# Performance work log

Measured on AMD Instinct MI355X. Metric: run time of the kernel, lower is better.

## Reference

```python
import jax, jax.numpy as jnp
import numpy as np

L, D, FF, V, B, S, H, GS = 6, 1024, 4096, 32000, 2, 1024, 16, 128
DH = D // H


def setup_inputs() -> dict:
    key = jax.random.key(0)
    ks = jax.random.split(key, 32)

    def tern(k, shape):
        # ternary values in {-1, 0, 1}, stored as float32 (int8 buffer in torch)
        return jax.random.randint(k, shape, -1, 2).astype(jnp.float32)

    def sc(k, shape):
        # positive per-group scales (abs-mean init, clamped > 0)
        return jax.random.uniform(k, shape, jnp.float32, 0.01, 0.1)

    inp = {
        'input_ids': jax.random.randint(ks[0], (B, S), 0, V),
        'emb_t': tern(ks[1], (V, D)),
        'emb_s': sc(ks[2], (V * D // GS,)),
        'pos_emb': jax.random.normal(ks[3], (S, D), jnp.float32) * 0.02,
        'q_t': tern(ks[4], (L, D, D)), 'q_s': sc(ks[5], (L, D * D // GS)),
        'k_t': tern(ks[6], (L, D, D)), 'k_s': sc(ks[7], (L, D * D // GS)),
        'v_t': tern(ks[8], (L, D, D)), 'v_s': sc(ks[9], (L, D * D // GS)),
        'o_t': tern(ks[10], (L, D, D)), 'o_s': sc(ks[11], (L, D * D // GS)),
        'g_t': tern(ks[12], (L, FF, D)), 'g_s': sc(ks[13], (L, D * FF // GS)),
        'u_t': tern(ks[14], (L, FF, D)), 'u_s': sc(ks[15], (L, D * FF // GS)),
        'd_t': tern(ks[16], (L, D, FF)), 'd_s': sc(ks[17], (L, D * FF // GS)),
        'alpha': jnp.full((L, H, 1, 1), 0.1, jnp.float32),
        'na_w': jnp.ones((L, D), jnp.float32),
        'nm_w': jnp.ones((L, D), jnp.float32),
        'nf_w': jnp.ones((D,), jnp.float32),
        'head_t': tern(ks[18], (V, D)),
        'head_s': sc(ks[19], (V * D // GS,)),
    }
    return inp


def _dq(t, s):
    # dequantize: reshape ternary to (..., n_groups, GS), scale per group
    tg = t.reshape(t.shape[:-2] + (-1, GS))
    return (tg * s[..., :, None]).reshape(t.shape)


def _rms(x, w, eps=1e-6):
    return x * jax.lax.rsqrt(jnp.mean(x * x, axis=-1, keepdims=True) + eps) * w


def _forward(input_ids, emb_t, emb_s, pos_emb, q_t, q_s, k_t, k_s, v_t, v_s,
             o_t, o_s, g_t, g_s, u_t, u_s, d_t, d_s, alpha, na_w, nm_w, nf_w,
             head_t, head_s):
    x = _dq(emb_t, emb_s)[input_ids] + pos_emb[None, :S]  # [B,S,D]
    causal = jnp.tril(jnp.ones((S, S), bool))
    scale = DH ** -0.5

    def block(x, p):
        (qt, qs, kt, ks_, vt, vs, ot, os_, gt, gs_, ut, us, dt, ds,
         al, naw, nmw) = p
        h = _rms(x, naw)

        def proj(t, s):
            return (h @ _dq(t, s).T).reshape(B, S, H, DH).transpose(0, 2, 1, 3)

        q, k, v = proj(qt, qs), proj(kt, ks_), proj(vt, vs)
        att = jnp.einsum('bhqd,bhkd->bhqk', q, k) * scale
        att = jax.nn.softmax(jnp.where(causal, att, -jnp.inf), axis=-1)
        out = jnp.einsum('bhqk,bhkd->bhqd', att, v)
        # residual head-mix: out += alpha * x_heads (x here is the normed input h)
        out = out + al * h.reshape(B, S, H, DH).transpose(0, 2, 1, 3)
        out = out.transpose(0, 2, 1, 3).reshape(B, S, D)
        x = x + out @ _dq(ot, os_).T
        h2 = _rms(x, nmw)
        gate = h2 @ _dq(gt, gs_).T
        up = h2 @ _dq(ut, us).T
        x = x + (jax.nn.silu(gate) * up) @ _dq(dt, ds).T
        return x, None

    params = (q_t, q_s, k_t, k_s, v_t, v_s, o_t, o_s, g_t, g_s, u_t, u_s,
              d_t, d_s, alpha, na_w, nm_w)
    x, _ = jax.lax.scan(block, x, params)
    x = _rms(x, nf_w)
    return x @ _dq(head_t, head_s).T  # [B,S,V]


def reference(input_ids, emb_t, emb_s, pos_emb, q_t, q_s, k_t, k_s, v_t, v_s,
              o_t, o_s, g_t, g_s, u_t, u_s, d_t, d_s, alpha, na_w, nm_w, nf_w,
              head_t, head_s):
    return _forward(input_ids, emb_t, emb_s, pos_emb, q_t, q_s, k_t, k_s,
                    v_t, v_s, o_t, o_s, g_t, g_s, u_t, u_s, d_t, d_s,
                    alpha, na_w, nm_w, nf_w, head_t, head_s)
```

## Files before the change

kernel.cpp:

```cpp
#include <hip/hip_runtime.h>
#include <math.h>

#define Lc   6
#define Dc   1024
#define FFc  4096
#define Vc   32000
#define Bc   2
#define Sc   1024
#define Hc   16
#define GSc  128
#define DHc  64
#define Mc   (Bc * Sc)

typedef __attribute__((ext_vector_type(8))) short bf16x8;
typedef __attribute__((ext_vector_type(4))) float f32x4;

__device__ inline unsigned ph2(float a, float b) {
    return (__float_as_uint(b) & 0xffff0000u) | (__float_as_uint(a) >> 16);
}
__device__ inline float flo(float a) {
    return a - __uint_as_float(__float_as_uint(a) & 0xffff0000u);
}
__device__ inline ushort bhi(float a) { return (ushort)(__float_as_uint(a) >> 16); }
__device__ inline ushort blo(float a) { return (ushort)(__float_as_uint(flo(a)) >> 16); }
__device__ inline float unbf(ushort h) { return __uint_as_float((unsigned)h << 16); }

__device__ inline size_t swz_bidx(int row, int col, int K) {
    size_t byte = (size_t)col * 2;
    size_t base = (size_t)row * K * 2 + (byte & ~(size_t)127);
    int inner = (int)(byte & 127);
    inner = (inner & 15) | ((((inner >> 4) ^ (row & 7)) & 7) << 4);
    return base + (size_t)inner;
}

__device__ inline void glds16(const void* g, void* l) {
    __builtin_amdgcn_global_load_lds(
        (const __attribute__((address_space(1))) void*)g,
        (__attribute__((address_space(3))) void*)l, 16, 0, 0);
}

__device__ inline float block_reduce_sum(float v, float* scratch) {
    __syncthreads();
    int lane = threadIdx.x & 63, w = threadIdx.x >> 6;
#pragma unroll
    for (int off = 32; off > 0; off >>= 1) v += __shfl_down(v, off, 64);
    if (lane == 0) scratch[w] = v;
    __syncthreads();
    if (threadIdx.x == 0) scratch[0] = scratch[0] + scratch[1] + scratch[2] + scratch[3];
    __syncthreads();
    return scratch[0];
}

__global__ __launch_bounds__(256) void k_embed(const int* __restrict__ ids,
                                               const float* __restrict__ et,
                                               const float* __restrict__ es,
                                               const float* __restrict__ pos,
                                               float* __restrict__ x) {
    int row = blockIdx.x;
    int sp  = row & (Sc - 1);
    int d   = threadIdx.x << 2;
    int idx = ids[row];
    int base = idx * Dc + d;
    float4 t = *(const float4*)(et + base);
    float  s = es[base >> 7];
    float4 p = *(const float4*)(pos + sp * Dc + d);
    float4 o;
    o.x = fmaf(t.x, s, p.x); o.y = fmaf(t.y, s, p.y);
    o.z = fmaf(t.z, s, p.z); o.w = fmaf(t.w, s, p.w);
    *(float4*)(x + row * Dc + d) = o;
}

__global__ __launch_bounds__(256) void k_rmsnorm_bf(const float* __restrict__ x,
                                                    const float* __restrict__ w,
                                                    ushort* __restrict__ hi,
                                                    ushort* __restrict__ lo) {
    __shared__ float scratch[4];
    int row = blockIdx.x;
    int d = threadIdx.x << 2;
    float4 f = *(const float4*)(x + (size_t)row * Dc + d);
    float s = f.x * f.x + f.y * f.y + f.z * f.z + f.w * f.w;
    s = block_reduce_sum(s, scratch);
    float rinv = rsqrtf(s * (1.0f / Dc) + 1e-6f);
    float4 wv = *(const float4*)(w + d);
    float o0 = f.x * rinv * wv.x, o1 = f.y * rinv * wv.y;
    float o2 = f.z * rinv * wv.z, o3 = f.w * rinv * wv.w;
    ushort4 hv, lv;
    hv.x = bhi(o0); hv.y = bhi(o1); hv.z = bhi(o2); hv.w = bhi(o3);
    lv.x = blo(o0); lv.y = blo(o1); lv.z = blo(o2); lv.w = blo(o3);
    const size_t sb = swz_bidx(row, d, Dc);
    *(ushort4*)((char*)hi + sb) = hv;
    *(ushort4*)((char*)lo + sb) = lv;
}

template <bool RESID>
__device__ __forceinline__ void gemm_core(
    const ushort* __restrict__ Ahi, const ushort* __restrict__ Alo,
    const float* __restrict__ Wt, const float* __restrict__ Ws,
    const float* __restrict__ R, float* __restrict__ C,
    const int bn, const int N, const int K, const int g0, const int g1) {
    __shared__ char Ah[16384];
    __shared__ char Al[16384];
    __shared__ char Bh[16384];
    __shared__ float Wsl[128];

    const int tid  = threadIdx.x;
    const int lane = tid & 63;
    const int wv   = tid >> 6;
    const int wm   = (wv >> 1) << 6;
    const int wn   = (wv & 1) << 6;
    const int bm   = blockIdx.x << 7;
    const int kg   = K >> 7;

    const int sr   = tid >> 1;
    const int sh   = tid & 1;
    const int swr  = (sr & 7) << 4;
    const int rowb = sr << 7;
    const int colb = sh << 6;
    const float* Bbase = Wt + (size_t)(bn + sr) * K + (sh << 5);

    const int gr = (wv << 3) + (lane >> 3);
    const int gc = (lane & 7) << 4;
    const char* Abh = (const char*)Ahi;
    const char* Abl = (const char*)Alo;

    const int lr  = lane & 15;
    const int lkb = (lane >> 4) << 4;
    const int frs = (lane & 7) << 4;

    f32x4 acc[4][4], accg[4][4];
#pragma unroll
    for (int i = 0; i < 4; ++i)
#pragma unroll
        for (int j = 0; j < 4; ++j) {
            acc[i][j]  = (f32x4){0.f, 0.f, 0.f, 0.f};
            accg[i][j] = (f32x4){0.f, 0.f, 0.f, 0.f};
        }

    float4 bv[8];
    const int s0 = g0 << 1, s1 = g1 << 1;
    {
        const float4* p = (const float4*)(Bbase + (s0 << 6));
#pragma unroll
        for (int jj = 0; jj < 8; ++jj) bv[jj] = p[jj];
    }

    for (int s = s0; s < s1; ++s) {
        const int k0 = s << 6;
        __syncthreads();
#pragma unroll
        for (int i = 0; i < 4; ++i) {
            const size_t sb = ((size_t)(bm + gr + (i << 5)) * K + k0) * 2 + gc;
            glds16(Abh + sb, Ah + (wv << 10) + (i << 12));
            glds16(Abl + sb, Al + (wv << 10) + (i << 12));
        }
        if ((s & 1) == 0 && tid < 128)
            Wsl[tid] = Ws[(size_t)(bn + tid) * kg + (s >> 1)];
#pragma unroll
        for (int j = 0; j < 4; ++j) {
            const int ob = rowb + ((colb + (j << 4)) ^ swr);
            float4 x0 = bv[2 * j], x1 = bv[2 * j + 1];
            *(uint4*)(Bh + ob) = make_uint4(ph2(x0.x, x0.y), ph2(x0.z, x0.w),
                                            ph2(x1.x, x1.y), ph2(x1.z, x1.w));
        }
        __syncthreads();
        if (s + 1 < s1) {
            const float4* p = (const float4*)(Bbase + ((s + 1) << 6));
#pragma unroll
            for (int jj = 0; jj < 8; ++jj) bv[jj] = p[jj];
        }
#pragma unroll
        for (int ks = 0; ks < 2; ++ks) {
            bf16x8 fa[4], fl[4], fb[4];
            const int cb = ((ks << 6) + lkb) ^ frs;
#pragma unroll
            for (int f = 0; f < 4; ++f) {
                const int ra = (wm + (f << 4) + lr) << 7;
                fa[f] = *(const bf16x8*)(Ah + ra + cb);
                fl[f] = *(const bf16x8*)(Al + ra + cb);
                const int rb = (wn + (f << 4) + lr) << 7;
                fb[f] = *(const bf16x8*)(Bh + rb + cb);
            }
#pragma unroll
            for (int i = 0; i < 4; ++i)
#pragma unroll
                for (int j = 0; j < 4; ++j) {
                    accg[i][j] = __builtin_amdgcn_mfma_f32_16x16x32_bf16(fa[i], fb[j], accg[i][j], 0, 0, 0);
                    accg[i][j] = __builtin_amdgcn_mfma_f32_16x16x32_bf16(fl[i], fb[j], accg[i][j], 0, 0, 0);
                }
        }
        if (s & 1) {
            float sv[4];
#pragma unroll
            for (int j = 0; j < 4; ++j) sv[j] = Wsl[wn + (j << 4) + lr];
#pragma unroll
            for (int i = 0; i < 4; ++i)
#pragma unroll
                for (int j = 0; j < 4; ++j) {
                    acc[i][j] += accg[i][j] * sv[j];
                    accg[i][j] = (f32x4){0.f, 0.f, 0.f, 0.f};
                }
        }
    }

    const int r0 = bm + wm + ((lane >> 4) << 2);
    const int c0 = bn + wn + lr;
#pragma unroll
    for (int i = 0; i < 4; ++i) {
        const int row = r0 + (i << 4);
#pragma unroll
        for (int j = 0; j < 4; ++j) {
            size_t off = (size_t)row * N + c0 + (j << 4);
#pragma unroll
            for (int e = 0; e < 4; ++e) {
                float vv = acc[i][j][e];
                if (RESID) vv += R[off];
                C[off] = vv;
                off += (size_t)N;
            }
        }
    }
}

template <bool RESID>
__global__ __launch_bounds__(256, 2) void k_gemm_bfa(
    const ushort* __restrict__ Ahi, const ushort* __restrict__ Alo,
    const float* __restrict__ Wt, const float* __restrict__ Ws,
    const float* __restrict__ R, float* __restrict__ C, int N, int K) {
    gemm_core<RESID>(Ahi, Alo, Wt, Ws, R, C, blockIdx.y << 7, N, K, 0, K >> 7);
}

__global__ __launch_bounds__(256, 2) void k_gemm_part(
    const ushort* __restrict__ Ahi, const ushort* __restrict__ Alo,
    const float* __restrict__ Wt, const float* __restrict__ Ws,
    float* __restrict__ P, int N, int K, int gper) {
    const int z = blockIdx.z;
    gemm_core<false>(Ahi, Alo, Wt, Ws, nullptr, P + (size_t)z * Mc * Dc,
                     blockIdx.y << 7, N, K, z * gper, (z + 1) * gper);
}

__global__ __launch_bounds__(256, 2) void k_gemm_qkv(
    const ushort* __restrict__ Ahi, const ushort* __restrict__ Alo,
    const float* __restrict__ qt, const float* __restrict__ qs,
    const float* __restrict__ kt, const float* __restrict__ ks,
    const float* __restrict__ vt, const float* __restrict__ vs,
    float* __restrict__ qb, float* __restrict__ kb, float* __restrict__ vb) {
    const int which = blockIdx.y >> 3;
    const int bn = (blockIdx.y & 7) << 7;
    const float* Wt = which == 0 ? qt : which == 1 ? kt : vt;
    const float* Ws = which == 0 ? qs : which == 1 ? ks : vs;
    float* C = which == 0 ? qb : which == 1 ? kb : vb;
    gemm_core<false>(Ahi, Alo, Wt, Ws, nullptr, C, bn, Dc, Dc, 0, Dc >> 7);
}

__global__ __launch_bounds__(256, 2) void k_gemm_gu(
    const ushort* __restrict__ Ahi, const ushort* __restrict__ Alo,
    const float* __restrict__ gt, const float* __restrict__ gs,
    const float* __restrict__ ut, const float* __restrict__ us,
    float* __restrict__ gate, float* __restrict__ up) {
    const int which = blockIdx.y >> 5;
    const int bn = (blockIdx.y & 31) << 7;
    const float* Wt = which == 0 ? gt : ut;
    const float* Ws = which == 0 ? gs : us;
    float* C = which == 0 ? gate : up;
    gemm_core<false>(Ahi, Alo, Wt, Ws, nullptr, C, bn, FFc, Dc, 0, Dc >> 7);
}

__global__ __launch_bounds__(256) void k_red4(const float* __restrict__ p,
                                              float* __restrict__ x) {
    const size_t i = (((size_t)blockIdx.x << 8) + threadIdx.x) << 2;
    const size_t st = (size_t)Mc * Dc;
    float4 a  = *(const float4*)(x + i);
    float4 p0 = *(const float4*)(p + i);
    float4 p1 = *(const float4*)(p + i + st);
    float4 p2 = *(const float4*)(p + i + 2 * st);
    float4 p3 = *(const float4*)(p + i + 3 * st);
    a.x += p0.x + p1.x + p2.x + p3.x;
    a.y += p0.y + p1.y + p2.y + p3.y;
    a.z += p0.z + p1.z + p2.z + p3.z;
    a.w += p0.w + p1.w + p2.w + p3.w;
    *(float4*)(x + i) = a;
}

__global__ __launch_bounds__(256) void k_silumul(const float* __restrict__ g,
                                                 const float* __restrict__ u,
                                                 ushort* __restrict__ fhi,
                                                 ushort* __restrict__ fl2) {
    const size_t i = (((size_t)blockIdx.x << 8) + threadIdx.x) << 2;
    float4 gv = *(const float4*)(g + i);
    float4 uv = *(const float4*)(u + i);
    float r0 = uv.x * (gv.x / (1.0f + expf(-gv.x)));
    float r1 = uv.y * (gv.y / (1.0f + expf(-gv.y)));
    float r2 = uv.z * (gv.z / (1.0f + expf(-gv.z)));
    float r3 = uv.w * (gv.w / (1.0f + expf(-gv.w)));
    ushort4 hv, lv;
    hv.x = bhi(r0); hv.y = bhi(r1); hv.z = bhi(r2); hv.w = bhi(r3);
    lv.x = blo(r0); lv.y = blo(r1); lv.z = blo(r2); lv.w = blo(r3);
    const int row = (int)(i >> 12);
    const int col = (int)(i & 4095);
    const size_t sb = swz_bidx(row, col, FFc);
    *(ushort4*)((char*)fhi + sb) = hv;
    *(ushort4*)((char*)fl2 + sb) = lv;
}

__global__ __launch_bounds__(256, 2) void k_attn_mfma(
    const float* __restrict__ q, const float* __restrict__ k,
    const float* __restrict__ v, const ushort* __restrict__ hnhi,
    const ushort* __restrict__ hnlo, const float* __restrict__ alpha,
    ushort* __restrict__ aohi, ushort* __restrict__ aolo) {
    __shared__ uint4 KhV[512], KlV[512];
    __shared__ uint4 VthV[512], VtlV[512];
    __shared__ uint4 PhV[512], PlV[512];
    char* Khc  = (char*)KhV;
    char* Klc  = (char*)KlV;
    char* Vthc = (char*)VthV;
    char* Vtlc = (char*)VtlV;

    const int t = blockIdx.x, hh = blockIdx.y, b = blockIdx.z;
    const int tid  = threadIdx.x;
    const int lane = tid & 63, w = tid >> 6;
    const int lr = lane & 15, g = lane >> 4;
    const int bS = b * Sc;
    const int hoff = hh * DHc;

    char* myPh = (char*)PhV + (w << 11);
    char* myPl = (char*)PlV + (w << 11);

    const int qrow = (t << 6) + (w << 4) + lr;
    bf16x8 qh[2], ql[2];
    {
        const float* qp = q + (size_t)(bS + qrow) * Dc + hoff + (g << 3);
#pragma unroll
        for (int c = 0; c < 2; ++c) {
            float4 f0 = *(const float4*)(qp + (c << 5));
            float4 f1 = *(const float4*)(qp + (c << 5) + 4);
            float s[8] = {f0.x * 0.125f, f0.y * 0.125f, f0.z * 0.125f, f0.w * 0.125f,
                          f1.x * 0.125f, f1.y * 0.125f, f1.z * 0.125f, f1.w * 0.125f};
            union { bf16x8 v; unsigned u[4]; } Hh, Ll;
#pragma unroll
            for (int p = 0; p < 4; ++p) {
                Hh.u[p] = ph2(s[2 * p], s[2 * p + 1]);
                Ll.u[p] = ph2(flo(s[2 * p]), flo(s[2 * p + 1]));
            }
            qh[c] = Hh.v; ql[c] = Ll.v;
        }
    }

    f32x4 oacc[4];
    float m[4], lsum[4];
#pragma unroll
    for (int f = 0; f < 4; ++f) oacc[f] = (f32x4){0.f, 0.f, 0.f, 0.f};
#pragma unroll
    for (int e = 0; e < 4; ++e) { m[e] = -3.0e38f; lsum[e] = 0.f; }

    const int skey = tid >> 2, sseg = tid & 3;
    const int k4 = (tid >> 4) << 2, d4 = (tid & 15) << 2;

    float4 kr[4], vr[4];
    {
        const float* src = k + (size_t)(bS + skey) * Dc + hoff + (sseg << 4);
#pragma unroll
        for (int r = 0; r < 4; ++r) kr[r] = *(const float4*)(src + (r << 2));
        const float* vsrc = v + (size_t)(bS + k4) * Dc + hoff + d4;
#pragma unroll
        for (int r = 0; r < 4; ++r) vr[r] = *(const float4*)(vsrc + r * Dc);
    }

    const int nt = t + 1;
    for (int j = 0; j < nt; ++j) {
        {
            const int swz = (skey & 7) << 4;
            char* dsth = Khc + skey * 128;
            char* dstl = Klc + skey * 128;
            float4 a0 = kr[0], a1 = kr[1], a2 = kr[2], a3 = kr[3];
            *(uint4*)(dsth + (((sseg << 5)) ^ swz)) =
                make_uint4(ph2(a0.x, a0.y), ph2(a0.z, a0.w), ph2(a1.x, a1.y), ph2(a1.z, a1.w));
            *(uint4*)(dsth + (((sseg << 5) + 16) ^ swz)) =
                make_uint4(ph2(a2.x, a2.y), ph2(a2.z, a2.w), ph2(a3.x, a3.y), ph2(a3.z, a3.w));
            *(uint4*)(dstl + (((sseg << 5)) ^ swz)) =
                make_uint4(ph2(flo(a0.x), flo(a0.y)), ph2(flo(a0.z), flo(a0.w)),
                           ph2(flo(a1.x), flo(a1.y)), ph2(flo(a1.z), flo(a1.w)));
            *(uint4*)(dstl + (((sseg << 5) + 16) ^ swz)) =
                make_uint4(ph2(flo(a2.x), flo(a2.y)), ph2(flo(a2.z), flo(a2.w)),
                           ph2(flo(a3.x), flo(a3.y)), ph2(flo(a3.z), flo(a3.w)));
        }
        {
            union { float4 v4; float f[4]; } r0, r1, r2, r3;
            r0.v4 = vr[0]; r1.v4 = vr[1]; r2.v4 = vr[2]; r3.v4 = vr[3];
#pragma unroll
            for (int d = 0; d < 4; ++d) {
                const int dh = d4 + d;
                const int byt = dh * 128 + (((k4 << 1)) ^ ((dh & 7) << 4));
                float x0 = r0.f[d], x1 = r1.f[d], x2 = r2.f[d], x3 = r3.f[d];
                *(uint2*)(Vthc + byt) = make_uint2(ph2(x0, x1), ph2(x2, x3));
                *(uint2*)(Vtlc + byt) =
                    make_uint2(ph2(flo(x0), flo(x1)), ph2(flo(x2), flo(x3)));
            }
        }
        __syncthreads();
        if (j + 1 < nt) {
            const int kb2 = (j + 1) << 6;
            const float* src = k + (size_t)(bS + kb2 + skey) * Dc + hoff + (sseg << 4);
#pragma unroll
            for (int r = 0; r < 4; ++r) kr[r] = *(const float4*)(src + (r << 2));
            const float* vsrc = v + (size_t)(bS + kb2 + k4) * Dc + hoff + d4;
#pragma unroll
            for (int r = 0; r < 4; ++r) vr[r] = *(const float4*)(vsrc + r * Dc);
        }

        f32x4 sacc[4];
#pragma unroll
        for (int f = 0; f < 4; ++f) sacc[f] = (f32x4){0.f, 0.f, 0.f, 0.f};
#pragma unroll
        for (int c = 0; c < 2; ++c) {
            const int cb = (c << 6) + (g << 4);
#pragma unroll
            for (int f = 0; f < 4; ++f) {
                const int row = (f << 4) + lr;
                const int byt = row * 128 + (cb ^ ((row & 7) << 4));
                bf16x8 kh = *(const bf16x8*)(Khc + byt);
                bf16x8 kl = *(const bf16x8*)(Klc + byt);
                sacc[f] = __builtin_amdgcn_mfma_f32_16x16x32_bf16(qh[c], kh, sacc[f], 0, 0, 0);
                sacc[f] = __builtin_amdgcn_mfma_f32_16x16x32_bf16(ql[c], kh, sacc[f], 0, 0, 0);
                sacc[f] = __builtin_amdgcn_mfma_f32_16x16x32_bf16(qh[c], kl, sacc[f], 0, 0, 0);
            }
        }
        if (j == t) {
            const int qloc = (w << 4) + (g << 2);
#pragma unroll
            for (int f = 0; f < 4; ++f) {
                const int key = (f << 4) + lr;
#pragma unroll
                for (int e = 0; e < 4; ++e)
                    if (key > qloc + e) sacc[f][e] = -3.0e38f;
            }
        }
        float rmax[4], corr[4], rsum[4];
#pragma unroll
        for (int e = 0; e < 4; ++e)
            rmax[e] = fmaxf(fmaxf(sacc[0][e], sacc[1][e]), fmaxf(sacc[2][e], sacc[3][e]));
#pragma unroll
        for (int msk = 1; msk <= 8; msk <<= 1)
#pragma unroll
            for (int e = 0; e < 4; ++e)
                rmax[e] = fmaxf(rmax[e], __shfl_xor(rmax[e], msk, 64));
#pragma unroll
        for (int e = 0; e < 4; ++e) {
            float mn = fmaxf(m[e], rmax[e]);
            corr[e] = __expf(m[e] - mn);
            m[e] = mn;
            rsum[e] = 0.f;
        }
#pragma unroll
        for (int f = 0; f < 4; ++f)
#pragma unroll
            for (int e = 0; e < 4; ++e) {
                float p = __expf(sacc[f][e] - m[e]);
                sacc[f][e] = p;
                rsum[e] += p;
            }
#pragma unroll
        for (int msk = 1; msk <= 8; msk <<= 1)
#pragma unroll
            for (int e = 0; e < 4; ++e) rsum[e] += __shfl_xor(rsum[e], msk, 64);
#pragma unroll
        for (int e = 0; e < 4; ++e) lsum[e] = lsum[e] * corr[e] + rsum[e];
#pragma unroll
        for (int f = 0; f < 4; ++f)
#pragma unroll
            for (int e = 0; e < 4; ++e) oacc[f][e] *= corr[e];

#pragma unroll
        for (int f = 0; f < 4; ++f) {
            const int key2 = ((f << 4) + lr) << 1;
#pragma unroll
            for (int e = 0; e < 4; ++e) {
                const int qr = (g << 2) + e;
                const int byt = qr * 128 + (key2 ^ ((qr & 7) << 4));
                unsigned bits = __float_as_uint(sacc[f][e]);
                unsigned hib = bits & 0xffff0000u;
                *(short*)(myPh + byt) = (short)(hib >> 16);
                float lov = sacc[f][e] - __uint_as_float(hib);
                *(short*)(myPl + byt) = (short)(__float_as_uint(lov) >> 16);
            }
        }
#pragma unroll
        for (int c = 0; c < 2; ++c) {
            const int cb = (c << 6) + (g << 4);
            const int pbyt = lr * 128 + (cb ^ ((lr & 7) << 4));
            bf16x8 pah = *(const bf16x8*)(myPh + pbyt);
            bf16x8 pal = *(const bf16x8*)(myPl + pbyt);
#pragma unroll
            for (int f = 0; f < 4; ++f) {
                const int row = (f << 4) + lr;
                const int byt = row * 128 + (cb ^ ((row & 7) << 4));
                bf16x8 vbh = *(const bf16x8*)(Vthc + byt);
                bf16x8 vbl = *(const bf16x8*)(Vtlc + byt);
                oacc[f] = __builtin_amdgcn_mfma_f32_16x16x32_bf16(pah, vbh, oacc[f], 0, 0, 0);
                oacc[f] = __builtin_amdgcn_mfma_f32_16x16x32_bf16(pal, vbh, oacc[f], 0, 0, 0);
                oacc[f] = __builtin_amdgcn_mfma_f32_16x16x32_bf16(pah, vbl, oacc[f], 0, 0, 0);
            }
        }
        __syncthreads();
    }

    const float al = alpha[hh];
    float invl[4];
#pragma unroll
    for (int e = 0; e < 4; ++e) invl[e] = 1.0f / lsum[e];
#pragma unroll
    for (int f = 0; f < 4; ++f) {
        const int dh = (f << 4) + lr;
#pragma unroll
        for (int e = 0; e < 4; ++e) {
            const int qg = (t << 6) + (w << 4) + (g << 2) + e;
            const int row = bS + qg;
            const size_t sb = swz_bidx(row, hoff + dh, Dc);
            float hnv = unbf(*(const ushort*)((const char*)hnhi + sb)) +
                        unbf(*(const ushort*)((const char*)hnlo + sb));
            float val = fmaf(al, hnv, oacc[f][e] * invl[e]);
            *(ushort*)((char*)aohi + sb) = bhi(val);
            *(ushort*)((char*)aolo + sb) = blo(val);
        }
    }
}

extern "C" void kernel_launch(void* const* d_in, const int* in_sizes, int n_in,
                              void* d_out, int out_size, void* d_ws, size_t ws_size,
                              hipStream_t stream) {
    const int*   ids    = (const int*)d_in[0];
    const float* emb_t  = (const float*)d_in[1];
    const float* emb_s  = (const float*)d_in[2];
    const float* pos    = (const float*)d_in[3];
    const float* q_t    = (const float*)d_in[4];
    const float* q_s    = (const float*)d_in[5];
    const float* k_t    = (const float*)d_in[6];
    const float* k_s    = (const float*)d_in[7];
    const float* v_t    = (const float*)d_in[8];
    const float* v_s    = (const float*)d_in[9];
    const float* o_t    = (const float*)d_in[10];
    const float* o_s    = (const float*)d_in[11];
    const float* g_t    = (const float*)d_in[12];
    const float* g_s    = (const float*)d_in[13];
    const float* u_t    = (const float*)d_in[14];
    const float* u_s    = (const float*)d_in[15];
    const float* dd_t   = (const float*)d_in[16];
    const float* dd_s   = (const float*)d_in[17];
    const float* alpha  = (const float*)d_in[18];
    const float* na_w   = (const float*)d_in[19];
    const float* nm_w   = (const float*)d_in[20];
    const float* nf_w   = (const float*)d_in[21];
    const float* head_t = (const float*)d_in[22];
    const float* head_s = (const float*)d_in[23];
    float* outp = (float*)d_out;

    float*  ws   = (float*)d_ws;
    float*  x    = ws;
    ushort* hhi  = (ushort*)(x + (size_t)Mc * Dc);
    ushort* hlo  = hhi + (size_t)Mc * Dc;
    float*  big  = (float*)(hlo + (size_t)Mc * Dc);
    float*  qb   = big;
    float*  kb   = big + (size_t)Mc * Dc;
    float*  vb   = big + (size_t)2 * Mc * Dc;
    ushort* aohi = (ushort*)(big + (size_t)3 * Mc * Dc);
    ushort* aolo = aohi + (size_t)Mc * Dc;
    float*  up   = big;
    float*  gate = (float*)d_out;
    ushort* ffhi = (ushort*)((char*)d_out + (size_t)Mc * FFc * 4);
    ushort* fflo = ffhi + (size_t)Mc * FFc;

    k_embed<<<Mc, 256, 0, stream>>>(ids, emb_t, emb_s, pos, x);

    const dim3 gD(Mc / 128, Dc / 128);
    const dim3 gQKV(Mc / 128, 3 * Dc / 128);
    const dim3 gGU(Mc / 128, 2 * FFc / 128);
    const dim3 gDN(Mc / 128, Dc / 128, 4);
    const dim3 gH(Mc / 128, Vc / 128);
    const dim3 gA(Sc / 64, Hc, Bc);
    const int  gSilu = (Mc * FFc) / (256 * 4);
    const int  gRed  = (Mc * Dc) / (256 * 4);

    for (int l = 0; l < Lc; ++l) {
        const float* qt = q_t + (size_t)l * Dc * Dc;
        const float* qs = q_s + (size_t)l * (Dc * Dc / GSc);
        const float* kt = k_t + (size_t)l * Dc * Dc;
        const float* ks = k_s + (size_t)l * (Dc * Dc / GSc);
        const float* vt = v_t + (size_t)l * Dc * Dc;
        const float* vs = v_s + (size_t)l * (Dc * Dc / GSc);
        const float* ot = o_t + (size_t)l * Dc * Dc;
        const float* os = o_s + (size_t)l * (Dc * Dc / GSc);
        const float* gt = g_t + (size_t)l * FFc * Dc;
        const float* gs = g_s + (size_t)l * (FFc * Dc / GSc);
        const float* ut = u_t + (size_t)l * FFc * Dc;
        const float* us = u_s + (size_t)l * (FFc * Dc / GSc);
        const float* dt = dd_t + (size_t)l * Dc * FFc;
        const float* ds = dd_s + (size_t)l * (Dc * FFc / GSc);

        k_rmsnorm_bf<<<Mc, 256, 0, stream>>>(x, na_w + l * Dc, hhi, hlo);
        k_gemm_qkv<<<gQKV, 256, 0, stream>>>(hhi, hlo, qt, qs, kt, ks, vt, vs, qb, kb, vb);
        k_attn_mfma<<<gA, 256, 0, stream>>>(qb, kb, vb, hhi, hlo, alpha + l * Hc, aohi, aolo);
        k_gemm_bfa<true><<<gD, 256, 0, stream>>>(aohi, aolo, ot, os, x, x, Dc, Dc);
        k_rmsnorm_bf<<<Mc, 256, 0, stream>>>(x, nm_w + l * Dc, hhi, hlo);
        k_gemm_gu<<<gGU, 256, 0, stream>>>(hhi, hlo, gt, gs, ut, us, gate, up);
        k_silumul<<<gSilu, 256, 0, stream>>>(gate, up, ffhi, fflo);
        k_gemm_part<<<gDN, 256, 0, stream>>>(ffhi, fflo, dt, ds, big, Dc, FFc, 8);
        k_red4<<<gRed, 256, 0, stream>>>(big, x);
    }

    k_rmsnorm_bf<<<Mc, 256, 0, stream>>>(x, nf_w, hhi, hlo);
    k_gemm_bfa<false><<<gH, 256, 0, stream>>>(hhi, hlo, head_t, head_s, nullptr, outp, Vc, Dc);
}
```

Measured before the change: 3.144 ms.

## Double-buffer GEMM LDS with 128x256 tiles, 512 threads and swizzled block order

Rewrites the shared GEMM core to use 512-thread blocks computing 128x256 tiles, with double-buffered LDS for A and B so the next k-step's loads overlap the current MFMA work and only one barrier is needed per step. Group scales are read directly into registers instead of through LDS, and a block-index swizzle reorders tiles to improve L2 reuse. The output projection now uses split-K partials plus the existing reduction kernel instead of a fused residual epilogue. The larger LDS footprint limits occupancy and adds an extra reduction pass for the O projection.

```diff
diff --git a/kernel.cpp b/kernel.cpp
--- a/kernel.cpp
+++ b/kernel.cpp
@@ -37,6 +37,15 @@
     __builtin_amdgcn_global_load_lds(
         (const __attribute__((address_space(1))) void*)g,
         (__attribute__((address_space(3))) void*)l, 16, 0, 0);
+}
+
+__device__ inline void swz_mt(int& m, int& t) {
+    const int nb  = gridDim.x * gridDim.y * gridDim.z;
+    const int bid = (blockIdx.z * gridDim.y + blockIdx.y) * gridDim.x + blockIdx.x;
+    const int q   = nb >> 3;
+    const int w   = (bid & 7) * q + (bid >> 3);
+    m = w & 15;
+    t = w >> 4;
 }
 
 __device__ inline float block_reduce_sum(float v, float* scratch) {
@@ -92,23 +101,21 @@
     *(ushort4*)((char*)lo + sb) = lv;
 }
 
-template <bool RESID>
-__device__ __forceinline__ void gemm_core(
+__device__ __forceinline__ void gemm_core2(
     const ushort* __restrict__ Ahi, const ushort* __restrict__ Alo,
     const float* __restrict__ Wt, const float* __restrict__ Ws,
-    const float* __restrict__ R, float* __restrict__ C,
-    const int bn, const int N, const int K, const int g0, const int g1) {
-    __shared__ char Ah[16384];
-    __shared__ char Al[16384];
-    __shared__ char Bh[16384];
-    __shared__ float Wsl[128];
+    float* __restrict__ C,
+    const int bm, const int bn, const int N, const int K,
+    const int g0, const int g1) {
+    __shared__ char AhB[32768];
+    __shared__ char AlB[32768];
+    __shared__ char BhB[65536];
 
     const int tid  = threadIdx.x;
     const int lane = tid & 63;
     const int wv   = tid >> 6;
-    const int wm   = (wv >> 1) << 6;
-    const int wn   = (wv & 1) << 6;
-    const int bm   = blockIdx.x << 7;
+    const int wm   = (wv & 1) << 6;
+    const int wn   = (wv >> 1) << 6;
     const int kg   = K >> 7;
 
     const int sr   = tid >> 1;
@@ -118,15 +125,21 @@
     const int colb = sh << 6;
     const float* Bbase = Wt + (size_t)(bn + sr) * K + (sh << 5);
 
-    const int gr = (wv << 3) + (lane >> 3);
-    const int gc = (lane & 7) << 4;
+    const int gr = tid >> 3;
+    const int gc = (tid & 7) << 4;
     const char* Abh = (const char*)Ahi;
     const char* Abl = (const char*)Alo;
+    const size_t K2 = (size_t)K * 2;
 
     const int lr  = lane & 15;
     const int lkb = (lane >> 4) << 4;
     const int frs = (lane & 7) << 4;
 
+    const float* Wsp[4];
+#pragma unroll
+    for (int j = 0; j < 4; ++j)
+        Wsp[j] = Ws + (size_t)(bn + wn + (j << 4) + lr) * kg;
+
     f32x4 acc[4][4], accg[4][4];
 #pragma unroll
     for (int i = 0; i < 4; ++i)
@@ -136,62 +149,86 @@
             accg[i][j] = (f32x4){0.f, 0.f, 0.f, 0.f};
         }
 
+    const int s0 = g0 << 1, s1 = g1 << 1;
     float4 bv[8];
-    const int s0 = g0 << 1, s1 = g1 << 1;
+    float  sv[4];
+
     {
-        const float4* p = (const float4*)(Bbase + (s0 << 6));
+        const int k0 = s0 << 6;
+#pragma unroll
+        for (int i = 0; i < 2; ++i) {
+            const size_t sb = (size_t)(bm + (i << 6) + gr) * K2 + ((size_t)k0 << 1) + gc;
+            glds16(Abh + sb, AhB + (i << 13) + (wv << 10));
+            glds16(Abl + sb, AlB + (i << 13) + (wv << 10));
+        }
+        const float4* p = (const float4*)(Bbase + k0);
 #pragma unroll
         for (int jj = 0; jj < 8; ++jj) bv[jj] = p[jj];
-    }
-
-    for (int s = s0; s < s1; ++s) {
-        const int k0 = s << 6;
-        __syncthreads();
-#pragma unroll
-        for (int i = 0; i < 4; ++i) {
-            const size_t sb = ((size_t)(bm + gr + (i << 5)) * K + k0) * 2 + gc;
-            glds16(Abh + sb, Ah + (wv << 10) + (i << 12));
-            glds16(Abl + sb, Al + (wv << 10) + (i << 12));
-        }
-        if ((s & 1) == 0 && tid < 128)
-            Wsl[tid] = Ws[(size_t)(bn + tid) * kg + (s >> 1)];
 #pragma unroll
         for (int j = 0; j < 4; ++j) {
             const int ob = rowb + ((colb + (j << 4)) ^ swr);
             float4 x0 = bv[2 * j], x1 = bv[2 * j + 1];
-            *(uint4*)(Bh + ob) = make_uint4(ph2(x0.x, x0.y), ph2(x0.z, x0.w),
-                                            ph2(x1.x, x1.y), ph2(x1.z, x1.w));
-        }
-        __syncthreads();
+            *(uint4*)(BhB + ob) = make_uint4(ph2(x0.x, x0.y), ph2(x0.z, x0.w),
+                                             ph2(x1.x, x1.y), ph2(x1.z, x1.w));
+        }
+    }
+    __syncthreads();
+
+    int cur = 0;
+    for (int s = s0; s < s1; ++s) {
+        const int nxt = cur ^ 1;
         if (s + 1 < s1) {
-            const float4* p = (const float4*)(Bbase + ((s + 1) << 6));
+            const int k0 = (s + 1) << 6;
+#pragma unroll
+            for (int i = 0; i < 2; ++i) {
+                const size_t sb = (size_t)(bm + (i << 6) + gr) * K2 + ((size_t)k0 << 1) + gc;
+                glds16(Abh + sb, AhB + (nxt << 14) + (i << 13) + (wv << 10));
+                glds16(Abl + sb, AlB + (nxt << 14) + (i << 13) + (wv << 10));
+            }
+            const float4* p = (const float4*)(Bbase + k0);
 #pragma unroll
             for (int jj = 0; jj < 8; ++jj) bv[jj] = p[jj];
         }
+        if ((s & 1) == 0) {
+#pragma unroll
+            for (int j = 0; j < 4; ++j) sv[j] = Wsp[j][s >> 1];
+        }
+
+        const char* AhC = AhB + (cur << 14);
+        const char* AlC = AlB + (cur << 14);
+        const char* BhC = BhB + (cur << 15);
 #pragma unroll
         for (int ks = 0; ks < 2; ++ks) {
-            bf16x8 fa[4], fl[4], fb[4];
             const int cb = ((ks << 6) + lkb) ^ frs;
+            bf16x8 fa[4], fl[4];
 #pragma unroll
             for (int f = 0; f < 4; ++f) {
                 const int ra = (wm + (f << 4) + lr) << 7;
-                fa[f] = *(const bf16x8*)(Ah + ra + cb);
-                fl[f] = *(const bf16x8*)(Al + ra + cb);
-                const int rb = (wn + (f << 4) + lr) << 7;
-                fb[f] = *(const bf16x8*)(Bh + rb + cb);
-            }
-#pragma unroll
-            for (int i = 0; i < 4; ++i)
-#pragma unroll
-                for (int j = 0; j < 4; ++j) {
-                    accg[i][j] = __builtin_amdgcn_mfma_f32_16x16x32_bf16(fa[i], fb[j], accg[i][j], 0, 0, 0);
-                    accg[i][j] = __builtin_amdgcn_mfma_f32_16x16x32_bf16(fl[i], fb[j], accg[i][j], 0, 0, 0);
+                fa[f] = *(const bf16x8*)(AhC + ra + cb);
+                fl[f] = *(const bf16x8*)(AlC + ra + cb);
+            }
+#pragma unroll
+            for (int j = 0; j < 4; ++j) {
+                const int rb = (wn + (j << 4) + lr) << 7;
+                bf16x8 fb = *(const bf16x8*)(BhC + rb + cb);
+#pragma unroll
+                for (int i = 0; i < 4; ++i) {
+                    accg[i][j] = __builtin_amdgcn_mfma_f32_16x16x32_bf16(fa[i], fb, accg[i][j], 0, 0, 0);
+                    accg[i][j] = __builtin_amdgcn_mfma_f32_16x16x32_bf16(fl[i], fb, accg[i][j], 0, 0, 0);
                 }
+            }
+        }
+        if (s + 1 < s1) {
+            char* BhN = BhB + (nxt << 15);
+#pragma unroll
+            for (int j = 0; j < 4; ++j) {
+                const int ob = rowb + ((colb + (j << 4)) ^ swr);
+                float4 x0 = bv[2 * j], x1 = bv[2 * j + 1];
+                *(uint4*)(BhN + ob) = make_uint4(ph2(x0.x, x0.y), ph2(x0.z, x0.w),
+                                                 ph2(x1.x, x1.y), ph2(x1.z, x1.w));
+            }
         }
         if (s & 1) {
-            float sv[4];
-#pragma unroll
-            for (int j = 0; j < 4; ++j) sv[j] = Wsl[wn + (j << 4) + lr];
 #pragma unroll
             for (int i = 0; i < 4; ++i)
 #pragma unroll
@@ -200,6 +237,8 @@
                     accg[i][j] = (f32x4){0.f, 0.f, 0.f, 0.f};
                 }
         }
+        __syncthreads();
+        cur = nxt;
     }
 
     const int r0 = bm + wm + ((lane >> 4) << 2);
@@ -212,57 +251,58 @@
             size_t off = (size_t)row * N + c0 + (j << 4);
 #pragma unroll
             for (int e = 0; e < 4; ++e) {
-                float vv = acc[i][j][e];
-                if (RESID) vv += R[off];
-                C[off] = vv;
+                C[off] = acc[i][j][e];
                 off += (size_t)N;
             }
         }
     }
 }
 
-template <bool RESID>
-__global__ __launch_bounds__(256, 2) void k_gemm_bfa(
+__global__ __launch_bounds__(512, 2) void k_gemm_bfa(
     const ushort* __restrict__ Ahi, const ushort* __restrict__ Alo,
     const float* __restrict__ Wt, const float* __restrict__ Ws,
-    const float* __restrict__ R, float* __restrict__ C, int N, int K) {
-    gemm_core<RESID>(Ahi, Alo, Wt, Ws, R, C, blockIdx.y << 7, N, K, 0, K >> 7);
-}
-
-__global__ __launch_bounds__(256, 2) void k_gemm_part(
+    float* __restrict__ C, int N, int K) {
+    int m, t; swz_mt(m, t);
+    gemm_core2(Ahi, Alo, Wt, Ws, C, m << 7, t << 8, N, K, 0, K >> 7);
+}
+
+__global__ __launch_bounds__(512, 2) void k_gemm_part(
     const ushort* __restrict__ Ahi, const ushort* __restrict__ Alo,
     const float* __restrict__ Wt, const float* __restrict__ Ws,
-    float* __restrict__ P, int N, int K, int gper) {
-    const int z = blockIdx.z;
-    gemm_core<false>(Ahi, Alo, Wt, Ws, nullptr, P + (size_t)z * Mc * Dc,
-                     blockIdx.y << 7, N, K, z * gper, (z + 1) * gper);
-}
-
-__global__ __launch_bounds__(256, 2) void k_gemm_qkv(
+    float* __restrict__ P, int K, int gper) {
+    int m, t; swz_mt(m, t);
+    const int y = t & 3, z = t >> 2;
+    gemm_core2(Ahi, Alo, Wt, Ws, P + (size_t)z * Mc * Dc,
+               m << 7, y << 8, Dc, K, z * gper, (z + 1) * gper);
+}
+
+__global__ __launch_bounds__(512, 2) void k_gemm_qkv(
     const ushort* __restrict__ Ahi, const ushort* __restrict__ Alo,
     const float* __restrict__ qt, const float* __restrict__ qs,
     const float* __restrict__ kt, const float* __restrict__ ks,
     const float* __restrict__ vt, const float* __restrict__ vs,
     float* __restrict__ qb, float* __restrict__ kb, float* __restrict__ vb) {
-    const int which = blockIdx.y >> 3;
-    const int bn = (blockIdx.y & 7) << 7;
+    int m, t; swz_mt(m, t);
+    const int which = t >> 2;
+    const int bn = (t & 3) << 8;
     const float* Wt = which == 0 ? qt : which == 1 ? kt : vt;
     const float* Ws = which == 0 ? qs : which == 1 ? ks : vs;
     float* C = which == 0 ? qb : which == 1 ? kb : vb;
-    gemm_core<false>(Ahi, Alo, Wt, Ws, nullptr, C, bn, Dc, Dc, 0, Dc >> 7);
-}
-
-__global__ __launch_bounds__(256, 2) void k_gemm_gu(
+    gemm_core2(Ahi, Alo, Wt, Ws, C, m << 7, bn, Dc, Dc, 0, Dc >> 7);
+}
+
+__global__ __launch_bounds__(512, 2) void k_gemm_gu(
     const ushort* __restrict__ Ahi, const ushort* __restrict__ Alo,
     const float* __restrict__ gt, const float* __restrict__ gs,
     const float* __restrict__ ut, const float* __restrict__ us,
     float* __restrict__ gate, float* __restrict__ up) {
-    const int which = blockIdx.y >> 5;
-    const int bn = (blockIdx.y & 31) << 7;
+    int m, t; swz_mt(m, t);
+    const int which = t >> 4;
+    const int bn = (t & 15) << 8;
     const float* Wt = which == 0 ? gt : ut;
     const float* Ws = which == 0 ? gs : us;
     float* C = which == 0 ? gate : up;
-    gemm_core<false>(Ahi, Alo, Wt, Ws, nullptr, C, bn, FFc, Dc, 0, Dc >> 7);
+    gemm_core2(Ahi, Alo, Wt, Ws, C, m << 7, bn, FFc, Dc, 0, Dc >> 7);
 }
 
 __global__ __launch_bounds__(256) void k_red4(const float* __restrict__ p,
@@ -565,16 +605,16 @@
     ushort* aolo = aohi + (size_t)Mc * Dc;
     float*  up   = big;
     float*  gate = (float*)d_out;
+    float*  part = (float*)d_out;
     ushort* ffhi = (ushort*)((char*)d_out + (size_t)Mc * FFc * 4);
     ushort* fflo = ffhi + (size_t)Mc * FFc;
 
     k_embed<<<Mc, 256, 0, stream>>>(ids, emb_t, emb_s, pos, x);
 
-    const dim3 gD(Mc / 128, Dc / 128);
-    const dim3 gQKV(Mc / 128, 3 * Dc / 128);
-    const dim3 gGU(Mc / 128, 2 * FFc / 128);
-    const dim3 gDN(Mc / 128, Dc / 128, 4);
-    const dim3 gH(Mc / 128, Vc / 128);
+    const dim3 gQKV(Mc / 128, 12);
+    const dim3 gGU(Mc / 128, 32);
+    const dim3 gSK(Mc / 128, 4, 4);
+    const dim3 gH(Mc / 128, Vc / 256);
     const dim3 gA(Sc / 64, Hc, Bc);
     const int  gSilu = (Mc * FFc) / (256 * 4);
     const int  gRed  = (Mc * Dc) / (256 * 4);
@@ -596,16 +636,17 @@
         const float* ds = dd_s + (size_t)l * (Dc * FFc / GSc);
 
         k_rmsnorm_bf<<<Mc, 256, 0, stream>>>(x, na_w + l * Dc, hhi, hlo);
-        k_gemm_qkv<<<gQKV, 256, 0, stream>>>(hhi, hlo, qt, qs, kt, ks, vt, vs, qb, kb, vb);
+        k_gemm_qkv<<<gQKV, 512, 0, stream>>>(hhi, hlo, qt, qs, kt, ks, vt, vs, qb, kb, vb);
         k_attn_mfma<<<gA, 256, 0, stream>>>(qb, kb, vb, hhi, hlo, alpha + l * Hc, aohi, aolo);
-        k_gemm_bfa<true><<<gD, 256, 0, stream>>>(aohi, aolo, ot, os, x, x, Dc, Dc);
+        k_gemm_part<<<gSK, 512, 0, stream>>>(aohi, aolo, ot, os, part, Dc, 2);
+        k_red4<<<gRed, 256, 0, stream>>>(part, x);
         k_rmsnorm_bf<<<Mc, 256, 0, stream>>>(x, nm_w + l * Dc, hhi, hlo);
-        k_gemm_gu<<<gGU, 256, 0, stream>>>(hhi, hlo, gt, gs, ut, us, gate, up);
+        k_gemm_gu<<<gGU, 512, 0, stream>>>(hhi, hlo, gt, gs, ut, us, gate, up);
         k_silumul<<<gSilu, 256, 0, stream>>>(gate, up, ffhi, fflo);
-        k_gemm_part<<<gDN, 256, 0, stream>>>(ffhi, fflo, dt, ds, big, Dc, FFc, 8);
-        k_red4<<<gRed, 256, 0, stream>>>(big, x);
+        k_gemm_part<<<gSK, 512, 0, stream>>>(ffhi, fflo, dt, ds, part, FFc, 8);
+        k_red4<<<gRed, 256, 0, stream>>>(part, x);
     }
 
     k_rmsnorm_bf<<<Mc, 256, 0, stream>>>(x, nf_w, hhi, hlo);
-    k_gemm_bfa<false><<<gH, 256, 0, stream>>>(hhi, hlo, head_t, head_s, nullptr, outp, Vc, Dc);
-}
+    k_gemm_bfa<<<gH, 512, 0, stream>>>(hhi, hlo, head_t, head_s, outp, Vc, Dc);
+}
```

Result: slower. 3.589 ms (+14.2%).

## Swizzle GEMM block order, split-K the O-projection, raise occupancy to 3

Applied to the files above, without the earlier changes.

Adds a block-index remap that spreads consecutive block ids across chunks of the grid, so blocks running at the same time share weight tiles across the 16 M-tiles and L2 reuse improves. The O-projection now uses 4-way split-K partial GEMMs plus the reduce kernel instead of a single residual GEMM, which gives it more blocks to fill the GPU. Launch bounds go from 2 to 3 blocks per CU. The cost is extra partial-sum traffic and one more kernel launch per layer, plus tighter register limits that may cause spills.

```diff
diff --git a/kernel.cpp b/kernel.cpp
--- a/kernel.cpp
+++ b/kernel.cpp
@@ -37,6 +37,15 @@
     __builtin_amdgcn_global_load_lds(
         (const __attribute__((address_space(1))) void*)g,
         (__attribute__((address_space(3))) void*)l, 16, 0, 0);
+}
+
+__device__ inline void swz_mt(int& m, int& t) {
+    const int nb  = gridDim.x * gridDim.y * gridDim.z;
+    const int bid = (blockIdx.z * gridDim.y + blockIdx.y) * gridDim.x + blockIdx.x;
+    const int q   = nb >> 3;
+    const int w   = (bid & 7) * q + (bid >> 3);
+    m = w & 15;
+    t = w >> 4;
 }
 
 __device__ inline float block_reduce_sum(float v, float* scratch) {
@@ -97,7 +106,8 @@
     const ushort* __restrict__ Ahi, const ushort* __restrict__ Alo,
     const float* __restrict__ Wt, const float* __restrict__ Ws,
     const float* __restrict__ R, float* __restrict__ C,
-    const int bn, const int N, const int K, const int g0, const int g1) {
+    const int bm, const int bn, const int N, const int K,
+    const int g0, const int g1) {
     __shared__ char Ah[16384];
     __shared__ char Al[16384];
     __shared__ char Bh[16384];
@@ -108,7 +118,6 @@
     const int wv   = tid >> 6;
     const int wm   = (wv >> 1) << 6;
     const int wn   = (wv & 1) << 6;
-    const int bm   = blockIdx.x << 7;
     const int kg   = K >> 7;
 
     const int sr   = tid >> 1;
@@ -221,48 +230,51 @@
     }
 }
 
-template <bool RESID>
-__global__ __launch_bounds__(256, 2) void k_gemm_bfa(
+__global__ __launch_bounds__(256, 3) void k_gemm_head(
     const ushort* __restrict__ Ahi, const ushort* __restrict__ Alo,
     const float* __restrict__ Wt, const float* __restrict__ Ws,
-    const float* __restrict__ R, float* __restrict__ C, int N, int K) {
-    gemm_core<RESID>(Ahi, Alo, Wt, Ws, R, C, blockIdx.y << 7, N, K, 0, K >> 7);
-}
-
-__global__ __launch_bounds__(256, 2) void k_gemm_part(
+    float* __restrict__ C, int N, int K) {
+    int m, t; swz_mt(m, t);
+    gemm_core<false>(Ahi, Alo, Wt, Ws, nullptr, C, m << 7, t << 7, N, K, 0, K >> 7);
+}
+
+__global__ __launch_bounds__(256, 3) void k_gemm_part(
     const ushort* __restrict__ Ahi, const ushort* __restrict__ Alo,
     const float* __restrict__ Wt, const float* __restrict__ Ws,
-    float* __restrict__ P, int N, int K, int gper) {
-    const int z = blockIdx.z;
+    float* __restrict__ P, int K, int gper) {
+    int m, t; swz_mt(m, t);
+    const int y = t & 7, z = t >> 3;
     gemm_core<false>(Ahi, Alo, Wt, Ws, nullptr, P + (size_t)z * Mc * Dc,
-                     blockIdx.y << 7, N, K, z * gper, (z + 1) * gper);
-}
-
-__global__ __launch_bounds__(256, 2) void k_gemm_qkv(
+                     m << 7, y << 7, Dc, K, z * gper, (z + 1) * gper);
+}
+
+__global__ __launch_bounds__(256, 3) void k_gemm_qkv(
     const ushort* __restrict__ Ahi, const ushort* __restrict__ Alo,
     const float* __restrict__ qt, const float* __restrict__ qs,
     const float* __restrict__ kt, const float* __restrict__ ks,
     const float* __restrict__ vt, const float* __restrict__ vs,
     float* __restrict__ qb, float* __restrict__ kb, float* __restrict__ vb) {
-    const int which = blockIdx.y >> 3;
-    const int bn = (blockIdx.y & 7) << 7;
+    int m, t; swz_mt(m, t);
+    const int which = t >> 3;
+    const int bn = (t & 7) << 7;
     const float* Wt = which == 0 ? qt : which == 1 ? kt : vt;
     const float* Ws = which == 0 ? qs : which == 1 ? ks : vs;
     float* C = which == 0 ? qb : which == 1 ? kb : vb;
-    gemm_core<false>(Ahi, Alo, Wt, Ws, nullptr, C, bn, Dc, Dc, 0, Dc >> 7);
-}
-
-__global__ __launch_bounds__(256, 2) void k_gemm_gu(
+    gemm_core<false>(Ahi, Alo, Wt, Ws, nullptr, C, m << 7, bn, Dc, Dc, 0, Dc >> 7);
+}
+
+__global__ __launch_bounds__(256, 3) void k_gemm_gu(
     const ushort* __restrict__ Ahi, const ushort* __restrict__ Alo,
     const float* __restrict__ gt, const float* __restrict__ gs,
     const float* __restrict__ ut, const float* __restrict__ us,
     float* __restrict__ gate, float* __restrict__ up) {
-    const int which = blockIdx.y >> 5;
-    const int bn = (blockIdx.y & 31) << 7;
+    int m, t; swz_mt(m, t);
+    const int which = t >> 5;
+    const int bn = (t & 31) << 7;
     const float* Wt = which == 0 ? gt : ut;
     const float* Ws = which == 0 ? gs : us;
     float* C = which == 0 ? gate : up;
-    gemm_core<false>(Ahi, Alo, Wt, Ws, nullptr, C, bn, FFc, Dc, 0, Dc >> 7);
+    gemm_core<false>(Ahi, Alo, Wt, Ws, nullptr, C, m << 7, bn, FFc, Dc, 0, Dc >> 7);
 }
 
 __global__ __launch_bounds__(256) void k_red4(const float* __restrict__ p,
@@ -565,15 +577,15 @@
     ushort* aolo = aohi + (size_t)Mc * Dc;
     float*  up   = big;
     float*  gate = (float*)d_out;
+    float*  part = (float*)d_out;
     ushort* ffhi = (ushort*)((char*)d_out + (size_t)Mc * FFc * 4);
     ushort* fflo = ffhi + (size_t)Mc * FFc;
 
     k_embed<<<Mc, 256, 0, stream>>>(ids, emb_t, emb_s, pos, x);
 
-    const dim3 gD(Mc / 128, Dc / 128);
-    const dim3 gQKV(Mc / 128, 3 * Dc / 128);
-    const dim3 gGU(Mc / 128, 2 * FFc / 128);
-    const dim3 gDN(Mc / 128, Dc / 128, 4);
+    const dim3 gQKV(Mc / 128, 24);
+    const dim3 gGU(Mc / 128, 64);
+    const dim3 gSK(Mc / 128, 8, 4);
     const dim3 gH(Mc / 128, Vc / 128);
     const dim3 gA(Sc / 64, Hc, Bc);
     const int  gSilu = (Mc * FFc) / (256 * 4);
@@ -598,14 +610,15 @@
         k_rmsnorm_bf<<<Mc, 256, 0, stream>>>(x, na_w + l * Dc, hhi, hlo);
         k_gemm_qkv<<<gQKV, 256, 0, stream>>>(hhi, hlo, qt, qs, kt, ks, vt, vs, qb, kb, vb);
         k_attn_mfma<<<gA, 256, 0, stream>>>(qb, kb, vb, hhi, hlo, alpha + l * Hc, aohi, aolo);
-        k_gemm_bfa<true><<<gD, 256, 0, stream>>>(aohi, aolo, ot, os, x, x, Dc, Dc);
+        k_gemm_part<<<gSK, 256, 0, stream>>>(aohi, aolo, ot, os, part, Dc, 2);
+        k_red4<<<gRed, 256, 0, stream>>>(part, x);
         k_rmsnorm_bf<<<Mc, 256, 0, stream>>>(x, nm_w + l * Dc, hhi, hlo);
         k_gemm_gu<<<gGU, 256, 0, stream>>>(hhi, hlo, gt, gs, ut, us, gate, up);
         k_silumul<<<gSilu, 256, 0, stream>>>(gate, up, ffhi, fflo);
-        k_gemm_part<<<gDN, 256, 0, stream>>>(ffhi, fflo, dt, ds, big, Dc, FFc, 8);
-        k_red4<<<gRed, 256, 0, stream>>>(big, x);
+        k_gemm_part<<<gSK, 256, 0, stream>>>(ffhi, fflo, dt, ds, part, FFc, 8);
+        k_red4<<<gRed, 256, 0, stream>>>(part, x);
     }
 
     k_rmsnorm_bf<<<Mc, 256, 0, stream>>>(x, nf_w, hhi, hlo);
-    k_gemm_bfa<false><<<gH, 256, 0, stream>>>(hhi, hlo, head_t, head_s, nullptr, outp, Vc, Dc);
-}
+    k_gemm_head<<<gH, 256, 0, stream>>>(hhi, hlo, head_t, head_s, outp, Vc, Dc);
+}
```

After: 4.812 ms. 53.1% more time.
